# Optimization experiments

Hardware: AMD Instinct MI355X
Metric: run time of the kernel (lower is better)

The kernel has to match this reference:

```python
import jax, jax.numpy as jnp
import numpy as np

B, T, H = 1024, 1024, 64


def _lstm_cell(x, h, c, w_ih, w_hh, b_ih, b_hh):
    # gates: [B, 4H] in PyTorch order i, f, g, o
    g = x @ w_ih.T + h @ w_hh.T + b_ih + b_hh
    i, f, gg, o = jnp.split(g, 4, axis=-1)
    i = jax.nn.sigmoid(i)
    f = jax.nn.sigmoid(f)
    gg = jnp.tanh(gg)
    o = jax.nn.sigmoid(o)
    c_new = f * c + i * gg
    h_new = o * jnp.tanh(c_new)
    return h_new, c_new


def setup_inputs() -> dict:
    key = jax.random.key(0)
    ks = jax.random.split(key, 12)
    s = 1.0 / np.sqrt(H)  # torch default init scale
    r = lambda k, shape: jax.random.normal(k, shape, dtype=jnp.float32) * s
    return {
        "x": jax.random.normal(ks[0], (B, T), dtype=jnp.float32),
        "w_ih1": r(ks[1], (4 * H, 1)),
        "w_hh1": r(ks[2], (4 * H, H)),
        "b_ih1": r(ks[3], (4 * H,)),
        "b_hh1": r(ks[4], (4 * H,)),
        "w_ih2": r(ks[5], (4 * H, H)),
        "w_hh2": r(ks[6], (4 * H, H)),
        "b_ih2": r(ks[7], (4 * H,)),
        "b_hh2": r(ks[8], (4 * H,)),
        "w_lin": r(ks[9], (1, H)),
        "b_lin": r(ks[10], (1,)),
        "future_preds": 0,
    }


def reference(x, w_ih1, w_hh1, b_ih1, b_hh1, w_ih2, w_hh2, b_ih2, b_hh2,
              w_lin, b_lin, future_preds):
    bsz = x.shape[0]
    h1 = jnp.zeros((bsz, H), x.dtype)
    c1 = jnp.zeros((bsz, H), x.dtype)
    h2 = jnp.zeros((bsz, H), x.dtype)
    c2 = jnp.zeros((bsz, H), x.dtype)

    def step(carry, x_t):
        h1, c1, h2, c2 = carry
        h1, c1 = _lstm_cell(x_t, h1, c1, w_ih1, w_hh1, b_ih1, b_hh1)
        h2, c2 = _lstm_cell(h1, h2, c2, w_ih2, w_hh2, b_ih2, b_hh2)
        out = h2 @ w_lin.T + b_lin  # [B, 1]
        return (h1, c1, h2, c2), out

    xs = x.T[:, :, None]  # [T, B, 1]
    carry, outs = jax.lax.scan(step, (h1, c1, h2, c2), xs)
    outputs = outs[:, :, 0].T  # [B, T]

    if future_preds > 0:
        last = outs[-1]  # [B, 1]

        def fstep(carry, _):
            h1, c1, h2, c2, prev = carry
            h1, c1 = _lstm_cell(prev, h1, c1, w_ih1, w_hh1, b_ih1, b_hh1)
            h2, c2 = _lstm_cell(h1, h2, c2, w_ih2, w_hh2, b_ih2, b_hh2)
            out = h2 @ w_lin.T + b_lin
            return (h1, c1, h2, c2, out), out

        _, fouts = jax.lax.scan(fstep, (*carry, last), None, length=future_preds)
        outputs = jnp.concatenate([outputs, fouts[:, :, 0].T], axis=1)

    return outputs
```

## Files before the change

### kernel.cpp

```cpp
#include <hip/hip_runtime.h>
#include <hip/hip_bf16.h>


typedef _Float16 f16x8 __attribute__((ext_vector_type(8)));
typedef float    f32x4 __attribute__((ext_vector_type(4)));

namespace {
constexpr int Bb = 1024;
constexpr int Tt = 1024;
constexpr int NBat = 4;
constexpr int HSTR = 72;
constexpr int XSTR = 1025;

__device__ __forceinline__ int srow(int row) {
    return row ^ ((row >> 3) & 7);
}
__device__ __forceinline__ float sigm_pre(float a) {
    return __builtin_amdgcn_rcpf(1.0f + __builtin_amdgcn_exp2f(a));
}
__device__ __forceinline__ float tanh_pre(float a) {
    return fmaf(2.0f, __builtin_amdgcn_rcpf(1.0f + __builtin_amdgcn_exp2f(a)), -1.0f);
}
__device__ __forceinline__ float tanh_f(float x) {
    float e = __builtin_amdgcn_exp2f(-2.8853900817779268f * x);
    return fmaf(2.0f, __builtin_amdgcn_rcpf(1.0f + e), -1.0f);
}
template <int CTRL>
__device__ __forceinline__ float dpp_sum_step(float p) {
    int v = __builtin_amdgcn_update_dpp(0, __float_as_int(p), CTRL, 0xf, 0xf, true);
    return p + __int_as_float(v);
}
__device__ __forceinline__ bool detect_f32(const void* w) {
    const unsigned short* p = (const unsigned short*)w;
    int sane = 0;
    for (int i = 0; i < 64; ++i) {
        int e = (p[2 * i] >> 7) & 0xFF;
        if (e >= 107 && e <= 129) ++sane;
    }
    return sane < 32;
}
__device__ __forceinline__ float ld(const void* p, int i, bool f32) {
    return f32 ? ((const float*)p)[i]
               : __bfloat162float(((const __hip_bfloat16*)p)[i]);
}
__device__ __forceinline__ void st(void* p, int i, float v, bool f32) {
    if (f32) ((float*)p)[i] = v;
    else     ((__hip_bfloat16*)p)[i] = __float2bfloat16(v);
}
}

__global__ __launch_bounds__(512, 1) void lstm2_kernel(
    const void* __restrict__ x,
    const void* __restrict__ w_ih1,
    const void* __restrict__ w_hh1,
    const void* __restrict__ b_ih1,
    const void* __restrict__ b_hh1,
    const void* __restrict__ w_ih2,
    const void* __restrict__ w_hh2,
    const void* __restrict__ b_ih2,
    const void* __restrict__ b_hh2,
    const void* __restrict__ w_lin,
    const void* __restrict__ b_lin,
    void* __restrict__ out)
{
    const int tid  = threadIdx.x;
    const int lane = tid & 63;
    const int w    = tid >> 6;
    const int gw   = w & 3;
    const bool isP = w < 4;
    const int m    = lane & 15;
    const int quad = lane >> 4;
    const int bb   = blockIdx.x * NBat;

    const bool f32 = detect_f32(w_hh1);

    __shared__ float                  xs[NBat * XSTR];
    __shared__ __align__(16) _Float16 h1buf[2][16 * HSTR];
    __shared__ __align__(16) _Float16 h2buf[2][16 * HSTR];
    __shared__ __align__(16) float    scr1[4][64 * 4];
    __shared__ __align__(16) float    scr2[4][64 * 4];
    __shared__ float                  headl[2][16];
    __shared__ float                  outbuf[NBat * Tt];

    for (int i = tid; i < NBat * 1024; i += 512)
        xs[(i >> 10) * XSTR + (i & 1023)] = ld(x, (bb + (i >> 10)) * Tt + (i & 1023), f32);
    for (int i = tid; i < 16 * HSTR; i += 512) {
        h1buf[0][i] = (_Float16)0; h1buf[1][i] = (_Float16)0;
        h2buf[0][i] = (_Float16)0; h2buf[1][i] = (_Float16)0;
    }

    const int arow = lane & 15;
    const int g_ld = arow & 3;
    const int u_ld = arow >> 2;
    const float scA = (g_ld == 2) ? -2.8853900817779268f : -1.4426950408889634f;
    f16x8 wfA[4][2], wfB[4][2];
    {
        const void* MA = isP ? w_hh1 : w_ih2;
#pragma unroll
        for (int q = 0; q < 4; ++q) {
            const int row = 64 * g_ld + 16 * gw + 4 * q + u_ld;
#pragma unroll
            for (int s = 0; s < 2; ++s) {
                const int base = row * 64 + 32 * s + quad * 8;
                if (f32) {
                    const float* A = (const float*)MA;
                    const float* B = (const float*)w_hh2;
#pragma unroll
                    for (int j = 0; j < 8; ++j) {
                        wfA[q][s][j] = (_Float16)(scA * A[base + j]);
                        wfB[q][s][j] = isP ? (_Float16)0.0f
                                           : (_Float16)(scA * B[base + j]);
                    }
                } else {
                    const __hip_bfloat16* A = (const __hip_bfloat16*)MA;
                    const __hip_bfloat16* B = (const __hip_bfloat16*)w_hh2;
#pragma unroll
                    for (int j = 0; j < 8; ++j) {
                        wfA[q][s][j] = (_Float16)(scA * __bfloat162float(A[base + j]));
                        wfB[q][s][j] = isP ? (_Float16)0.0f
                                           : (_Float16)(scA * __bfloat162float(B[base + j]));
                    }
                }
            }
        }
    }
    f32x4 bv[4], wxv[4];
#pragma unroll
    for (int q = 0; q < 4; ++q)
#pragma unroll
        for (int r = 0; r < 4; ++r) {
            const int row = 64 * r + 16 * gw + 4 * q + quad;
            const float sg = (r == 2) ? -2.8853900817779268f : -1.4426950408889634f;
            bv[q][r] = sg * (isP ? (ld(b_ih1, row, f32) + ld(b_hh1, row, f32))
                                 : (ld(b_ih2, row, f32) + ld(b_hh2, row, f32)));
            wxv[q][r] = isP ? sg * ld(w_ih1, row, f32) : 0.0f;
        }
    const int cb = lane >> 4;
    const int uo = lane & 15;
    const int cidx = srow(lane) * 4;
    int swadr[4];
#pragma unroll
    for (int q = 0; q < 4; ++q) swadr[q] = srow(m * 16 + q * 4 + quad) * 4;
    const float wl_u = ld(w_lin, 16 * gw + uo, f32);
    const float blin = ld(b_lin, 0, f32);
    float cst = 0.0f;
    f16x8 pa0{}, pa1{}, pb0{}, pb1{};
    __syncthreads();

#pragma unroll 2
    for (int t = 0; t <= Tt; ++t) {
        if (isP) {
            if (t < Tt) {
                f32x4 acc[4];
                const float xt = xs[(m & (NBat - 1)) * XSTR + t];
#pragma unroll
                for (int q = 0; q < 4; ++q)
#pragma unroll
                    for (int r = 0; r < 4; ++r)
                        acc[q][r] = fmaf(xt, wxv[q][r], bv[q][r]);
                if (t > 0) {
                    const _Float16* hp = h1buf[(t - 1) & 1] + m * HSTR;
                    if (m < NBat) {
                        pa0 = *(const f16x8*)(hp + quad * 8);
                        pa1 = *(const f16x8*)(hp + 32 + quad * 8);
                    }
                    __builtin_amdgcn_s_setprio(1);
#pragma unroll
                    for (int q = 0; q < 4; ++q) {
                        acc[q] = __builtin_amdgcn_mfma_f32_16x16x32_f16(wfA[q][0], pa0, acc[q], 0, 0, 0);
                        acc[q] = __builtin_amdgcn_mfma_f32_16x16x32_f16(wfA[q][1], pa1, acc[q], 0, 0, 0);
                    }
                    __builtin_amdgcn_s_setprio(0);
                }
                if (m < NBat)
#pragma unroll
                    for (int q = 0; q < 4; ++q)
                        *(f32x4*)&scr1[gw][swadr[q]] = acc[q];
                const f32x4 g = *(const f32x4*)&scr1[gw][cidx];
                float ig = sigm_pre(g[0]), fg = sigm_pre(g[1]);
                float gg = tanh_pre(g[2]), og = sigm_pre(g[3]);
                cst = fmaf(fg, cst, ig * gg);
                h1buf[t & 1][cb * HSTR + 16 * gw + uo] = (_Float16)(og * tanh_f(cst));
            }
        } else {
            if (t > 0) {
                if (t > 1 && w == 4 && lane < NBat) {
                    float s = blin;
#pragma unroll
                    for (int k = 0; k < 4; ++k) s += headl[t & 1][k * 4 + lane];
                    outbuf[lane * Tt + (t - 2)] = s;
                }
                const _Float16* h1p = h1buf[(t - 1) & 1] + m * HSTR;
                const _Float16* h2p = h2buf[t & 1] + m * HSTR;
                if (m < NBat) {
                    pa0 = *(const f16x8*)(h1p + quad * 8);
                    pa1 = *(const f16x8*)(h1p + 32 + quad * 8);
                    pb0 = *(const f16x8*)(h2p + quad * 8);
                    pb1 = *(const f16x8*)(h2p + 32 + quad * 8);
                }
                f32x4 acc[4];
                __builtin_amdgcn_s_setprio(1);
#pragma unroll
                for (int q = 0; q < 4; ++q) {
                    f32x4 p2 = __builtin_amdgcn_mfma_f32_16x16x32_f16(wfA[q][0], pa0, bv[q], 0, 0, 0);
                    p2 = __builtin_amdgcn_mfma_f32_16x16x32_f16(wfA[q][1], pa1, p2, 0, 0, 0);
                    f32x4 p3 = __builtin_amdgcn_mfma_f32_16x16x32_f16(wfB[q][0], pb0, f32x4{0,0,0,0}, 0, 0, 0);
                    p3 = __builtin_amdgcn_mfma_f32_16x16x32_f16(wfB[q][1], pb1, p3, 0, 0, 0);
                    acc[q] = p2 + p3;
                }
                __builtin_amdgcn_s_setprio(0);
                if (m < NBat)
#pragma unroll
                    for (int q = 0; q < 4; ++q)
                        *(f32x4*)&scr2[gw][swadr[q]] = acc[q];
                const f32x4 g = *(const f32x4*)&scr2[gw][cidx];
                float ig = sigm_pre(g[0]), fg = sigm_pre(g[1]);
                float gg = tanh_pre(g[2]), og = sigm_pre(g[3]);
                cst = fmaf(fg, cst, ig * gg);
                float h = og * tanh_f(cst);
                h2buf[(t - 1) & 1][cb * HSTR + 16 * gw + uo] = (_Float16)h;
                float p = h * wl_u;
                p = dpp_sum_step<0x111>(p);
                p = dpp_sum_step<0x112>(p);
                p = dpp_sum_step<0x114>(p);
                p = dpp_sum_step<0x118>(p);
                if (uo == 15) headl[(t - 1) & 1][gw * 4 + cb] = p;
            }
        }
        __syncthreads();
    }

    if (w == 4 && lane < NBat) {
        float s = blin;
#pragma unroll
        for (int k = 0; k < 4; ++k) s += headl[(Tt - 1) & 1][k * 4 + lane];
        outbuf[lane * Tt + (Tt - 1)] = s;
    }
    __syncthreads();
    for (int i = tid; i < NBat * Tt; i += 512)
        st(out, (bb + (i >> 10)) * Tt + (i & 1023), outbuf[i], f32);
}

extern "C" void kernel_launch(void* const* d_in, const int* in_sizes, int n_in,
                              void* d_out, int out_size, void* d_ws, size_t ws_size,
                              hipStream_t stream)
{
    (void)in_sizes; (void)n_in; (void)out_size; (void)d_ws; (void)ws_size;
    lstm2_kernel<<<dim3(Bb / NBat), dim3(512), 0, stream>>>(
        d_in[0], d_in[1], d_in[2], d_in[3], d_in[4], d_in[5],
        d_in[6], d_in[7], d_in[8], d_in[9], d_in[10], d_out);
}
```

Baseline: 780.0 us.

## Replace per-step block barriers with LDS flag polling between layer warps

Drops the per-timestep __syncthreads that forced both LSTM layers to run in lockstep. Warps now signal progress through shared-memory step counters and spin-poll on them, and a 4-deep h1 ring buffer lets layer 1 run up to three steps ahead of layer 2. The aim is to decouple the two layers' critical paths and cut barrier stalls. The cost is spin-wait traffic on LDS, plus correctness that depends on the ordering of LDS writes and flag updates, which relies on only a compiler memory barrier.

```diff
diff --git a/kernel.cpp b/kernel.cpp
--- a/kernel.cpp
+++ b/kernel.cpp
@@ -46,6 +46,16 @@
 __device__ __forceinline__ void st(void* p, int i, float v, bool f32) {
     if (f32) ((float*)p)[i] = v;
     else     ((__hip_bfloat16*)p)[i] = __float2bfloat16(v);
+}
+__device__ __forceinline__ void poll_flags(const int* f, int tp, int tq, int lane) {
+    const int idx = lane & 7;
+    const int thr = (idx < 4) ? tp : tq;
+    for (;;) {
+        int v = ((const volatile int*)f)[idx];
+        if (__all(v >= thr)) break;
+    }
+    __builtin_amdgcn_sched_barrier(0);
+    asm volatile("" ::: "memory");
 }
 }
 
@@ -75,19 +85,22 @@
     const bool f32 = detect_f32(w_hh1);
 
     __shared__ float                  xs[NBat * XSTR];
-    __shared__ __align__(16) _Float16 h1buf[2][16 * HSTR];
+    __shared__ __align__(16) _Float16 h1ring[4][16 * HSTR];
     __shared__ __align__(16) _Float16 h2buf[2][16 * HSTR];
     __shared__ __align__(16) float    scr1[4][64 * 4];
     __shared__ __align__(16) float    scr2[4][64 * 4];
     __shared__ float                  headl[2][16];
     __shared__ float                  outbuf[NBat * Tt];
+    __shared__ int                    flg[8];
 
     for (int i = tid; i < NBat * 1024; i += 512)
         xs[(i >> 10) * XSTR + (i & 1023)] = ld(x, (bb + (i >> 10)) * Tt + (i & 1023), f32);
     for (int i = tid; i < 16 * HSTR; i += 512) {
-        h1buf[0][i] = (_Float16)0; h1buf[1][i] = (_Float16)0;
-        h2buf[0][i] = (_Float16)0; h2buf[1][i] = (_Float16)0;
-    }
+        h1ring[0][i] = (_Float16)0; h1ring[1][i] = (_Float16)0;
+        h1ring[2][i] = (_Float16)0; h1ring[3][i] = (_Float16)0;
+        h2buf[0][i] = (_Float16)0;  h2buf[1][i] = (_Float16)0;
+    }
+    if (tid < 8) flg[tid] = 0;
 
     const int arow = lane & 15;
     const int g_ld = arow & 3;
@@ -144,97 +157,108 @@
     const float wl_u = ld(w_lin, 16 * gw + uo, f32);
     const float blin = ld(b_lin, 0, f32);
     float cst = 0.0f;
-    f16x8 pa0{}, pa1{}, pb0{}, pb1{};
     __syncthreads();
 
-#pragma unroll 2
-    for (int t = 0; t <= Tt; ++t) {
-        if (isP) {
-            if (t < Tt) {
-                f32x4 acc[4];
-                const float xt = xs[(m & (NBat - 1)) * XSTR + t];
-#pragma unroll
-                for (int q = 0; q < 4; ++q)
-#pragma unroll
-                    for (int r = 0; r < 4; ++r)
-                        acc[q][r] = fmaf(xt, wxv[q][r], bv[q][r]);
-                if (t > 0) {
-                    const _Float16* hp = h1buf[(t - 1) & 1] + m * HSTR;
-                    if (m < NBat) {
-                        pa0 = *(const f16x8*)(hp + quad * 8);
-                        pa1 = *(const f16x8*)(hp + 32 + quad * 8);
-                    }
-                    __builtin_amdgcn_s_setprio(1);
-#pragma unroll
-                    for (int q = 0; q < 4; ++q) {
-                        acc[q] = __builtin_amdgcn_mfma_f32_16x16x32_f16(wfA[q][0], pa0, acc[q], 0, 0, 0);
-                        acc[q] = __builtin_amdgcn_mfma_f32_16x16x32_f16(wfA[q][1], pa1, acc[q], 0, 0, 0);
-                    }
-                    __builtin_amdgcn_s_setprio(0);
+    if (isP) {
+        f16x8 pa0{}, pa1{};
+#pragma unroll 4
+        for (int t = 0; t < Tt; ++t) {
+            poll_flags(flg, t, t - 3, lane);
+            f32x4 acc[4];
+            const float xt = xs[(m & (NBat - 1)) * XSTR + t];
+#pragma unroll
+            for (int q = 0; q < 4; ++q)
+#pragma unroll
+                for (int r = 0; r < 4; ++r)
+                    acc[q][r] = fmaf(xt, wxv[q][r], bv[q][r]);
+            if (t > 0) {
+                const _Float16* hp = h1ring[(t - 1) & 3] + m * HSTR;
+                if (m < NBat) {
+                    pa0 = *(const f16x8*)(hp + quad * 8);
+                    pa1 = *(const f16x8*)(hp + 32 + quad * 8);
                 }
-                if (m < NBat)
-#pragma unroll
-                    for (int q = 0; q < 4; ++q)
-                        *(f32x4*)&scr1[gw][swadr[q]] = acc[q];
-                const f32x4 g = *(const f32x4*)&scr1[gw][cidx];
-                float ig = sigm_pre(g[0]), fg = sigm_pre(g[1]);
-                float gg = tanh_pre(g[2]), og = sigm_pre(g[3]);
-                cst = fmaf(fg, cst, ig * gg);
-                h1buf[t & 1][cb * HSTR + 16 * gw + uo] = (_Float16)(og * tanh_f(cst));
-            }
-        } else {
-            if (t > 0) {
-                if (t > 1 && w == 4 && lane < NBat) {
-                    float s = blin;
-#pragma unroll
-                    for (int k = 0; k < 4; ++k) s += headl[t & 1][k * 4 + lane];
-                    outbuf[lane * Tt + (t - 2)] = s;
-                }
-                const _Float16* h1p = h1buf[(t - 1) & 1] + m * HSTR;
-                const _Float16* h2p = h2buf[t & 1] + m * HSTR;
-                if (m < NBat) {
-                    pa0 = *(const f16x8*)(h1p + quad * 8);
-                    pa1 = *(const f16x8*)(h1p + 32 + quad * 8);
-                    pb0 = *(const f16x8*)(h2p + quad * 8);
-                    pb1 = *(const f16x8*)(h2p + 32 + quad * 8);
-                }
-                f32x4 acc[4];
                 __builtin_amdgcn_s_setprio(1);
 #pragma unroll
                 for (int q = 0; q < 4; ++q) {
-                    f32x4 p2 = __builtin_amdgcn_mfma_f32_16x16x32_f16(wfA[q][0], pa0, bv[q], 0, 0, 0);
-                    p2 = __builtin_amdgcn_mfma_f32_16x16x32_f16(wfA[q][1], pa1, p2, 0, 0, 0);
-                    f32x4 p3 = __builtin_amdgcn_mfma_f32_16x16x32_f16(wfB[q][0], pb0, f32x4{0,0,0,0}, 0, 0, 0);
-                    p3 = __builtin_amdgcn_mfma_f32_16x16x32_f16(wfB[q][1], pb1, p3, 0, 0, 0);
-                    acc[q] = p2 + p3;
+                    acc[q] = __builtin_amdgcn_mfma_f32_16x16x32_f16(wfA[q][0], pa0, acc[q], 0, 0, 0);
+                    acc[q] = __builtin_amdgcn_mfma_f32_16x16x32_f16(wfA[q][1], pa1, acc[q], 0, 0, 0);
                 }
                 __builtin_amdgcn_s_setprio(0);
-                if (m < NBat)
-#pragma unroll
-                    for (int q = 0; q < 4; ++q)
-                        *(f32x4*)&scr2[gw][swadr[q]] = acc[q];
-                const f32x4 g = *(const f32x4*)&scr2[gw][cidx];
-                float ig = sigm_pre(g[0]), fg = sigm_pre(g[1]);
-                float gg = tanh_pre(g[2]), og = sigm_pre(g[3]);
-                cst = fmaf(fg, cst, ig * gg);
-                float h = og * tanh_f(cst);
-                h2buf[(t - 1) & 1][cb * HSTR + 16 * gw + uo] = (_Float16)h;
-                float p = h * wl_u;
-                p = dpp_sum_step<0x111>(p);
-                p = dpp_sum_step<0x112>(p);
-                p = dpp_sum_step<0x114>(p);
-                p = dpp_sum_step<0x118>(p);
-                if (uo == 15) headl[(t - 1) & 1][gw * 4 + cb] = p;
-            }
-        }
-        __syncthreads();
-    }
-
-    if (w == 4 && lane < NBat) {
-        float s = blin;
-#pragma unroll
-        for (int k = 0; k < 4; ++k) s += headl[(Tt - 1) & 1][k * 4 + lane];
-        outbuf[lane * Tt + (Tt - 1)] = s;
+            }
+            if (m < NBat)
+#pragma unroll
+                for (int q = 0; q < 4; ++q)
+                    *(f32x4*)&scr1[gw][swadr[q]] = acc[q];
+            const f32x4 g = *(const f32x4*)&scr1[gw][cidx];
+            float ig = sigm_pre(g[0]), fg = sigm_pre(g[1]);
+            float gg = tanh_pre(g[2]), og = sigm_pre(g[3]);
+            cst = fmaf(fg, cst, ig * gg);
+            h1ring[t & 3][cb * HSTR + 16 * gw + uo] = (_Float16)(og * tanh_f(cst));
+            if (lane == 0) {
+                asm volatile("" ::: "memory");
+                *(volatile int*)&flg[gw] = t + 1;
+            }
+        }
+    } else {
+        f16x8 pa0{}, pa1{}, pb0{}, pb1{};
+#pragma unroll 4
+        for (int u = 0; u < Tt; ++u) {
+            poll_flags(flg, u + 1, u, lane);
+            if (u > 0 && w == 4 && lane < NBat) {
+                float s = blin;
+#pragma unroll
+                for (int k = 0; k < 4; ++k) s += headl[(u - 1) & 1][k * 4 + lane];
+                outbuf[lane * Tt + (u - 1)] = s;
+            }
+            const _Float16* h1p = h1ring[u & 3] + m * HSTR;
+            const _Float16* h2p = h2buf[(u + 1) & 1] + m * HSTR;
+            if (m < NBat) {
+                pa0 = *(const f16x8*)(h1p + quad * 8);
+                pa1 = *(const f16x8*)(h1p + 32 + quad * 8);
+                pb0 = *(const f16x8*)(h2p + quad * 8);
+                pb1 = *(const f16x8*)(h2p + 32 + quad * 8);
+            }
+            f32x4 acc[4];
+            __builtin_amdgcn_s_setprio(1);
+#pragma unroll
+            for (int q = 0; q < 4; ++q) {
+                f32x4 p2 = __builtin_amdgcn_mfma_f32_16x16x32_f16(wfA[q][0], pa0, bv[q], 0, 0, 0);
+                p2 = __builtin_amdgcn_mfma_f32_16x16x32_f16(wfA[q][1], pa1, p2, 0, 0, 0);
+                f32x4 p3 = __builtin_amdgcn_mfma_f32_16x16x32_f16(wfB[q][0], pb0, f32x4{0,0,0,0}, 0, 0, 0);
+                p3 = __builtin_amdgcn_mfma_f32_16x16x32_f16(wfB[q][1], pb1, p3, 0, 0, 0);
+                acc[q] = p2 + p3;
+            }
+            __builtin_amdgcn_s_setprio(0);
+            if (m < NBat)
+#pragma unroll
+                for (int q = 0; q < 4; ++q)
+                    *(f32x4*)&scr2[gw][swadr[q]] = acc[q];
+            const f32x4 g = *(const f32x4*)&scr2[gw][cidx];
+            float ig = sigm_pre(g[0]), fg = sigm_pre(g[1]);
+            float gg = tanh_pre(g[2]), og = sigm_pre(g[3]);
+            cst = fmaf(fg, cst, ig * gg);
+            float h = og * tanh_f(cst);
+            h2buf[u & 1][cb * HSTR + 16 * gw + uo] = (_Float16)h;
+            float p = h * wl_u;
+            p = dpp_sum_step<0x111>(p);
+            p = dpp_sum_step<0x112>(p);
+            p = dpp_sum_step<0x114>(p);
+            p = dpp_sum_step<0x118>(p);
+            if (uo == 15) headl[u & 1][gw * 4 + cb] = p;
+            if (lane == 0) {
+                asm volatile("" ::: "memory");
+                *(volatile int*)&flg[4 + gw] = u + 1;
+            }
+        }
+        if (w == 4) {
+            poll_flags(flg, 0, Tt, lane);
+            if (lane < NBat) {
+                float s = blin;
+#pragma unroll
+                for (int k = 0; k < 4; ++k) s += headl[(Tt - 1) & 1][k * 4 + lane];
+                outbuf[lane * Tt + (Tt - 1)] = s;
+            }
+        }
     }
     __syncthreads();
     for (int i = tid; i < NBat * Tt; i += 512)
```

New measurement: 757.8 us. 2.8% less time.
